# Kernel optimization log

Hardware: AMD Instinct MI355X
Metric: run time of the kernel (lower is better)

## Reference

```python
import jax, jax.numpy as jnp
import numpy as np
from jax import lax

T, H, I, E = 1024, 2048, 1024, 16
G, TOPK_GROUP, TOP_K = 4, 2, 4
ROUTED_SCALE = 2.5
W_SCALE = 0.02  # keep activations in a sane range


def setup_inputs() -> dict:
    key = jax.random.key(0)
    ks = jax.random.split(key, 7)
    return {
        "hidden_states": jax.random.normal(ks[0], (T, H), jnp.float32),
        "gate_w": jax.random.normal(ks[1], (E, H), jnp.float32) * W_SCALE,
        "e_bias": jax.random.normal(ks[2], (E,), jnp.float32),
        "w_gate_up": jax.random.normal(ks[3], (E, 2 * I, H), jnp.float32) * W_SCALE,
        "w_down": jax.random.normal(ks[4], (E, H, I), jnp.float32) * W_SCALE,
        "shared_w_gate_up": jax.random.normal(ks[5], (2 * I, H), jnp.float32) * W_SCALE,
        "shared_w_down": jax.random.normal(ks[6], (H, I), jnp.float32) * W_SCALE,
    }


def _grouped_topk(scores, e_bias):
    # scores: sigmoid router scores [T, E]
    scores_b = scores + e_bias[None, :]
    # group score = sum of top-2 biased scores within each group (bias branch)
    group_scores = jnp.sum(lax.top_k(scores_b.reshape(-1, G, E // G), 2)[0], axis=-1)  # [T, G]
    _, group_idx = lax.top_k(group_scores, TOPK_GROUP)  # [T, topk_group]
    group_mask = jnp.any(jax.nn.one_hot(group_idx, G, dtype=jnp.bool_), axis=1)  # [T, G]
    score_mask = jnp.repeat(group_mask, E // G, axis=-1)  # [T, E]
    tmp = jnp.where(score_mask, scores_b, 0.0)
    _, topk_ids = lax.top_k(tmp, TOP_K)  # [T, K]
    topk_w = jnp.take_along_axis(scores, topk_ids, axis=1)  # weights from UNbiased scores
    topk_w = topk_w / jnp.sum(topk_w, axis=-1, keepdims=True)  # renormalize
    return topk_w, topk_ids


def _silu_and_mul(gu):
    g, u = jnp.split(gu, 2, axis=-1)
    return jax.nn.silu(g) * u


def reference(hidden_states, gate_w, e_bias, w_gate_up, w_down,
              shared_w_gate_up, shared_w_down):
    x = hidden_states  # [T, H]
    # shared expert MLP
    shared = _silu_and_mul(x @ shared_w_gate_up.T) @ shared_w_down.T  # [T, H]
    # router
    logits = x @ gate_w.T                      # [T, E]
    scores = jax.nn.sigmoid(logits)
    topk_w, topk_ids = _grouped_topk(scores, e_bias)
    # dense combine weights [T, E] (zero for unselected experts)
    combine = jnp.zeros((T, E), x.dtype).at[jnp.arange(T)[:, None], topk_ids].add(topk_w)
    # routed experts: SwiGLU per expert, combined with routing weights
    gu = jnp.einsum('th,eih->tei', x, w_gate_up)        # [T, E, 2I]
    a = _silu_and_mul(gu)                               # [T, E, I]
    routed = jnp.einsum('tei,ehi,te->th', a, w_down, combine)  # [T, H]
    return routed * ROUTED_SCALE + shared
```

## Files before the change

### kernel.cpp

```cpp
#include <hip/hip_runtime.h>
#include <math.h>

typedef __bf16 bf16;
typedef bf16 bf16x4 __attribute__((ext_vector_type(4)));
typedef bf16 bf16x8 __attribute__((ext_vector_type(8)));
typedef float f32x4 __attribute__((ext_vector_type(4)));

#define T_TOK   1024
#define H_DIM   2048
#define I_DIM   1024
#define E_NUM   16
#define NPAIR_R 4096
#define NPAIR   5120

typedef __attribute__((address_space(3))) unsigned int lds_uint;
typedef __attribute__((address_space(1))) const unsigned int gbl_uint;
__device__ __forceinline__ void gld16(const void* g, void* l) {
  __builtin_amdgcn_global_load_lds((gbl_uint*)g, (lds_uint*)l, 16, 0, 0);
}

__global__ __launch_bounds__(256) void router_kernel(
    const float* __restrict__ x, const float* __restrict__ gate_w,
    const float* __restrict__ e_bias, bf16* __restrict__ xb,
    float* __restrict__ out,
    int* __restrict__ topk_ids, float* __restrict__ topk_w,
    int* __restrict__ counts)
{
  int t = blockIdx.x;
  int tid = threadIdx.x;
  float acc[16];
#pragma unroll
  for (int e = 0; e < 16; ++e) acc[e] = 0.f;
  const float* xr = x + (size_t)t * H_DIM;
  bf16* xbr = xb + (size_t)t * H_DIM;
  float* outr = out + (size_t)t * H_DIM;
  for (int h = tid; h < H_DIM; h += 256) {
    float xv = xr[h];
    xbr[h] = (bf16)xv;
    outr[h] = 0.f;
#pragma unroll
    for (int e = 0; e < 16; ++e) acc[e] += xv * gate_w[e * H_DIM + h];
  }
#pragma unroll
  for (int e = 0; e < 16; ++e) {
#pragma unroll
    for (int off = 32; off >= 1; off >>= 1)
      acc[e] += __shfl_down(acc[e], off, 64);
  }
  __shared__ float red[4][16];
  int lane = tid & 63, wave = tid >> 6;
  if (lane == 0) {
#pragma unroll
    for (int e = 0; e < 16; ++e) red[wave][e] = acc[e];
  }
  __syncthreads();
  if (tid == 0) {
    float scores[16], sb[16];
    for (int e = 0; e < 16; ++e) {
      float l = red[0][e] + red[1][e] + red[2][e] + red[3][e];
      float s = 1.f / (1.f + expf(-l));
      scores[e] = s;
      sb[e] = s + e_bias[e];
    }
    float gs[4];
    for (int g = 0; g < 4; ++g) {
      float b1 = -1e30f, b2 = -1e30f;
      for (int j = 0; j < 4; ++j) {
        float v = sb[g * 4 + j];
        if (v > b1) { b2 = b1; b1 = v; }
        else if (v > b2) b2 = v;
      }
      gs[g] = b1 + b2;
    }
    int g1 = 0; float bv = gs[0];
    for (int g = 1; g < 4; ++g) if (gs[g] > bv) { bv = gs[g]; g1 = g; }
    int g2 = -1; float bv2 = -1e30f;
    for (int g = 0; g < 4; ++g) if (g != g1 && gs[g] > bv2) { bv2 = gs[g]; g2 = g; }
    float tmp[16];
    for (int e = 0; e < 16; ++e) {
      int grp = e >> 2;
      tmp[e] = (grp == g1 || grp == g2) ? sb[e] : 0.0f;
    }
    bool used[16] = {false};
    int ids[4]; float wv[4]; float wsum = 0.f;
    for (int k = 0; k < 4; ++k) {
      int bi = 0; float bvv = -1e30f;
      for (int i = 0; i < 16; ++i)
        if (!used[i] && tmp[i] > bvv) { bvv = tmp[i]; bi = i; }
      used[bi] = true;
      ids[k] = bi; wv[k] = scores[bi]; wsum += scores[bi];
    }
    float inv = 1.f / wsum;
    for (int k = 0; k < 4; ++k) {
      topk_ids[t * 4 + k] = ids[k];
      topk_w[t * 4 + k] = wv[k] * inv;
      atomicAdd(&counts[ids[k]], 1);
    }
  }
}

__global__ __launch_bounds__(1024) void build_pairs_kernel(
    const int* __restrict__ topk_ids, const float* __restrict__ topk_w,
    const int* __restrict__ counts, int* __restrict__ off,
    int* __restrict__ pair_token, float* __restrict__ pair_scale)
{
  __shared__ int s_off[17];
  __shared__ int s_cur[16];
  int tid = threadIdx.x;
  if (tid == 0) {
    int s = 0;
    for (int e = 0; e < 16; ++e) { s_off[e] = s; off[e] = s; s += counts[e]; }
    s_off[16] = s; off[16] = s;
  }
  if (tid < 16) s_cur[tid] = 0;
  __syncthreads();
  for (int i = tid; i < NPAIR; i += 1024) {
    if (i < NPAIR_R) {
      int e = topk_ids[i];
      int pos = atomicAdd(&s_cur[e], 1);
      int idx = s_off[e] + pos;
      pair_token[idx] = i >> 2;
      pair_scale[idx] = 2.5f * topk_w[i];
    } else {
      pair_token[i] = i - NPAIR_R;
      pair_scale[i] = 1.0f;
    }
  }
}

__global__ __launch_bounds__(256, 2) void gateup_kernel(
    const bf16* __restrict__ xb, const float* __restrict__ w_gu,
    const float* __restrict__ s_wgu,
    const int* __restrict__ off, const int* __restrict__ pair_token,
    bf16* __restrict__ a_buf)
{
  const int nt = blockIdx.x;
  const int mt = blockIdx.y;
  const int e  = blockIdx.z;
  const int poff = (e < 16) ? off[e]     : NPAIR_R;
  const int pend = (e < 16) ? off[e + 1] : NPAIR;
  const int cnt  = pend - poff;
  if (mt * 128 >= cnt) return;
  const float* __restrict__ B = (e < 16) ? (w_gu + (size_t)e * 2 * I_DIM * H_DIM) : s_wgu;

  __shared__ __align__(16) bf16  As[3 * 4096];
  __shared__ __align__(16) float Bs[3 * 4096];

  const int tid = threadIdx.x;
  const int lane = tid & 63;
  const int wave = tid >> 6;
  const int wm = wave >> 1, wn = wave & 1;
  const int c0 = lane >> 4;
  const int fr = lane & 15;

  const bf16* aptr[2];
#pragma unroll
  for (int s = 0; s < 2; ++s) {
    int idx = s * 256 + tid;
    int ar = idx >> 2, ach = idx & 3;
    int sch = ach ^ ((ar >> 1) & 3);
    int p = poff + mt * 128 + ar;
    aptr[s] = xb + (size_t)pair_token[p] * H_DIM + sch * 8;
  }
  const float* bptr[4];
#pragma unroll
  for (int s = 0; s < 4; ++s) {
    int idx = s * 256 + tid;
    int br = idx >> 3, bch = idx & 7;
    int sch = bch ^ (br & 7);
    int rg = nt * 64 + br + (br >= 64 ? 960 : 0);
    bptr[s] = B + (size_t)rg * H_DIM + sch * 4;
  }
  int a_off[4];
#pragma unroll
  for (int mi = 0; mi < 4; ++mi) {
    int ar = wm * 64 + mi * 16 + fr;
    a_off[mi] = ar * 64 + ((c0 ^ ((ar >> 1) & 3)) << 4);
  }
  int b_off[4];
#pragma unroll
  for (int ni = 0; ni < 4; ++ni) {
    int br = wn * 32 + (ni & 1) * 16 + fr + (ni >> 1) * 64;
    b_off[ni] = br * 128 + (((2 * c0) ^ (br & 7)) << 4);
  }

  f32x4 acc[4][4];
  f32x4 zz = {0.f, 0.f, 0.f, 0.f};
#pragma unroll
  for (int mi = 0; mi < 4; ++mi)
#pragma unroll
    for (int ni = 0; ni < 4; ++ni) acc[mi][ni] = zz;

  const int ldso = tid * 16;
  auto stage = [&](int k0, int b) {
#pragma unroll
    for (int s = 0; s < 2; ++s)
      gld16(aptr[s] + k0, (char*)As + b * 8192 + s * 4096 + ldso);
#pragma unroll
    for (int s = 0; s < 4; ++s)
      gld16(bptr[s] + k0, (char*)Bs + b * 16384 + s * 4096 + ldso);
  };
  auto compute = [&](int b) {
    const char* Ab = (const char*)As + b * 8192;
    const char* Bb = (const char*)Bs + b * 16384;
    bf16x8 af[4], bv[4];
#pragma unroll
    for (int mi = 0; mi < 4; ++mi)
      af[mi] = *(const bf16x8*)(Ab + a_off[mi]);
#pragma unroll
    for (int ni = 0; ni < 4; ++ni) {
      f32x4 x0 = *(const f32x4*)(Bb + b_off[ni]);
      f32x4 x1 = *(const f32x4*)(Bb + (b_off[ni] ^ 16));
      bf16x8 t;
      t[0] = (bf16)x0[0]; t[1] = (bf16)x0[1]; t[2] = (bf16)x0[2]; t[3] = (bf16)x0[3];
      t[4] = (bf16)x1[0]; t[5] = (bf16)x1[1]; t[6] = (bf16)x1[2]; t[7] = (bf16)x1[3];
      bv[ni] = t;
    }
#pragma unroll
    for (int mi = 0; mi < 4; ++mi)
#pragma unroll
      for (int ni = 0; ni < 4; ++ni)
        acc[mi][ni] = __builtin_amdgcn_mfma_f32_16x16x32_bf16(af[mi], bv[ni], acc[mi][ni], 0, 0, 0);
  };

  const int NT = H_DIM / 32;
  stage(0, 0);
  stage(32, 1);
  int ca = 0, cb = 1, cc = 2;
  for (int t = 0; t + 2 < NT; ++t) {
    stage((t + 2) * 32, cc);
    asm volatile("s_waitcnt vmcnt(12)" ::: "memory");
    __builtin_amdgcn_s_barrier();
    compute(ca);
    asm volatile("" ::: "memory");
    __builtin_amdgcn_s_barrier();
    int tmp = ca; ca = cb; cb = cc; cc = tmp;
  }
  asm volatile("s_waitcnt vmcnt(6)" ::: "memory");
  __builtin_amdgcn_s_barrier();
  compute(ca);
  asm volatile("s_waitcnt vmcnt(0)" ::: "memory");
  __builtin_amdgcn_s_barrier();
  compute(cb);

#pragma unroll
  for (int mi = 0; mi < 4; ++mi) {
#pragma unroll
    for (int reg = 0; reg < 4; ++reg) {
      int r = wm * 64 + mi * 16 + c0 * 4 + reg;
      int rl = mt * 128 + r;
      if (rl < cnt) {
        size_t p = (size_t)(poff + rl);
        bf16* orow = a_buf + p * I_DIM + nt * 64 + wn * 32 + fr;
#pragma unroll
        for (int ni = 0; ni < 2; ++ni) {
          float g = acc[mi][ni][reg];
          float u = acc[mi][ni + 2][reg];
          float sg = g / (1.f + expf(-g));
          orow[ni * 16] = (bf16)(sg * u);
        }
      }
    }
  }
}

__global__ __launch_bounds__(256, 2) void down_kernel(
    const bf16* __restrict__ a_buf, const float* __restrict__ w_dn,
    const float* __restrict__ s_wdn,
    const int* __restrict__ off, const int* __restrict__ pair_token,
    const float* __restrict__ pair_scale, float* __restrict__ out)
{
  const int nt = blockIdx.x;
  const int mt = blockIdx.y;
  const int e  = blockIdx.z;
  const int poff = (e < 16) ? off[e]     : NPAIR_R;
  const int pend = (e < 16) ? off[e + 1] : NPAIR;
  const int cnt  = pend - poff;
  if (mt * 128 >= cnt) return;
  const float* __restrict__ B = (e < 16) ? (w_dn + (size_t)e * H_DIM * I_DIM) : s_wdn;

  __shared__ __align__(16) bf16  As[3 * 4096];
  __shared__ __align__(16) float Bs[3 * 4096];

  const int tid = threadIdx.x;
  const int lane = tid & 63;
  const int wave = tid >> 6;
  const int wm = wave >> 1, wn = wave & 1;
  const int c0 = lane >> 4;
  const int fr = lane & 15;

  const bf16* aptr[2];
#pragma unroll
  for (int s = 0; s < 2; ++s) {
    int idx = s * 256 + tid;
    int ar = idx >> 2, ach = idx & 3;
    int sch = ach ^ ((ar >> 1) & 3);
    int p = poff + mt * 128 + ar;
    aptr[s] = a_buf + (size_t)p * I_DIM + sch * 8;
  }
  const float* bptr[4];
#pragma unroll
  for (int s = 0; s < 4; ++s) {
    int idx = s * 256 + tid;
    int br = idx >> 3, bch = idx & 7;
    int sch = bch ^ (br & 7);
    bptr[s] = B + (size_t)(nt * 128 + br) * I_DIM + sch * 4;
  }
  int a_off[4];
#pragma unroll
  for (int mi = 0; mi < 4; ++mi) {
    int ar = wm * 64 + mi * 16 + fr;
    a_off[mi] = ar * 64 + ((c0 ^ ((ar >> 1) & 3)) << 4);
  }
  int b_off[4];
#pragma unroll
  for (int ni = 0; ni < 4; ++ni) {
    int br = wn * 64 + ni * 16 + fr;
    b_off[ni] = br * 128 + (((2 * c0) ^ (br & 7)) << 4);
  }

  f32x4 acc[4][4];
  f32x4 zz = {0.f, 0.f, 0.f, 0.f};
#pragma unroll
  for (int mi = 0; mi < 4; ++mi)
#pragma unroll
    for (int ni = 0; ni < 4; ++ni) acc[mi][ni] = zz;

  const int ldso = tid * 16;
  auto stage = [&](int k0, int b) {
#pragma unroll
    for (int s = 0; s < 2; ++s)
      gld16(aptr[s] + k0, (char*)As + b * 8192 + s * 4096 + ldso);
#pragma unroll
    for (int s = 0; s < 4; ++s)
      gld16(bptr[s] + k0, (char*)Bs + b * 16384 + s * 4096 + ldso);
  };
  auto compute = [&](int b) {
    const char* Ab = (const char*)As + b * 8192;
    const char* Bb = (const char*)Bs + b * 16384;
    bf16x8 af[4], bv[4];
#pragma unroll
    for (int mi = 0; mi < 4; ++mi)
      af[mi] = *(const bf16x8*)(Ab + a_off[mi]);
#pragma unroll
    for (int ni = 0; ni < 4; ++ni) {
      f32x4 x0 = *(const f32x4*)(Bb + b_off[ni]);
      f32x4 x1 = *(const f32x4*)(Bb + (b_off[ni] ^ 16));
      bf16x8 t;
      t[0] = (bf16)x0[0]; t[1] = (bf16)x0[1]; t[2] = (bf16)x0[2]; t[3] = (bf16)x0[3];
      t[4] = (bf16)x1[0]; t[5] = (bf16)x1[1]; t[6] = (bf16)x1[2]; t[7] = (bf16)x1[3];
      bv[ni] = t;
    }
#pragma unroll
    for (int mi = 0; mi < 4; ++mi)
#pragma unroll
      for (int ni = 0; ni < 4; ++ni)
        acc[mi][ni] = __builtin_amdgcn_mfma_f32_16x16x32_bf16(af[mi], bv[ni], acc[mi][ni], 0, 0, 0);
  };

  const int NT = I_DIM / 32;
  stage(0, 0);
  stage(32, 1);
  int ca = 0, cb = 1, cc = 2;
  for (int t = 0; t + 2 < NT; ++t) {
    stage((t + 2) * 32, cc);
    asm volatile("s_waitcnt vmcnt(12)" ::: "memory");
    __builtin_amdgcn_s_barrier();
    compute(ca);
    asm volatile("" ::: "memory");
    __builtin_amdgcn_s_barrier();
    int tmp = ca; ca = cb; cb = cc; cc = tmp;
  }
  asm volatile("s_waitcnt vmcnt(6)" ::: "memory");
  __builtin_amdgcn_s_barrier();
  compute(ca);
  asm volatile("s_waitcnt vmcnt(0)" ::: "memory");
  __builtin_amdgcn_s_barrier();
  compute(cb);

  const int colb = nt * 128 + wn * 64;
#pragma unroll
  for (int mi = 0; mi < 4; ++mi) {
#pragma unroll
    for (int reg = 0; reg < 4; ++reg) {
      int r = wm * 64 + mi * 16 + c0 * 4 + reg;
      int rl = mt * 128 + r;
      if (rl < cnt) {
        int p = poff + rl;
        int tok = pair_token[p];
        float sc = pair_scale[p];
        float* orow = out + (size_t)tok * H_DIM + colb + fr;
#pragma unroll
        for (int ni = 0; ni < 4; ++ni)
          atomicAdd(&orow[ni * 16], acc[mi][ni][reg] * sc);
      }
    }
  }
}

extern "C" void kernel_launch(void* const* d_in, const int* in_sizes, int n_in,
                              void* d_out, int out_size, void* d_ws, size_t ws_size,
                              hipStream_t stream)
{
  const float* x     = (const float*)d_in[0];
  const float* gatew = (const float*)d_in[1];
  const float* ebias = (const float*)d_in[2];
  const float* w_gu  = (const float*)d_in[3];
  const float* w_dn  = (const float*)d_in[4];
  const float* s_wgu = (const float*)d_in[5];
  const float* s_wdn = (const float*)d_in[6];
  float* out = (float*)d_out;

  char* ws = (char*)d_ws;
  int*   off        = (int*)(ws + 0);
  int*   counts     = (int*)(ws + 128);
  int*   topk_ids   = (int*)(ws + 256);
  float* topk_w     = (float*)(ws + 16640);
  int*   pair_token = (int*)(ws + 33024);
  float* pair_scale = (float*)(ws + 53504);
  bf16*  x_bf16     = (bf16*)(ws + 73984);
  bf16*  a_buf      = (bf16*)(ws + 73984 + 4194304);

  hipMemsetAsync(ws + 128, 0, 64, stream);

  router_kernel<<<T_TOK, 256, 0, stream>>>(x, gatew, ebias, x_bf16, out,
                                           topk_ids, topk_w, counts);
  build_pairs_kernel<<<1, 1024, 0, stream>>>(topk_ids, topk_w, counts, off,
                                             pair_token, pair_scale);
  dim3 g1(16, 8, 17);
  gateup_kernel<<<g1, 256, 0, stream>>>(x_bf16, w_gu, s_wgu, off, pair_token, a_buf);
  dim3 g2(16, 8, 17);
  down_kernel<<<g2, 256, 0, stream>>>(a_buf, w_dn, s_wdn, off, pair_token, pair_scale, out);
}
```

Baseline: 666.4 us.

## Enlarge MoE GEMM M-tiles to 256 rows with 512-thread blocks and batch router tokens

The gate-up and down expert GEMMs now use 512-thread blocks that cover 256 pair rows instead of 128, and the pipeline drops from triple to double buffering. The grid is reordered so each expert's M-tiles are adjacent. Each fp32 weight tile is therefore loaded once per 256 rows rather than per 128, which roughly halves weight streaming from HBM. The router kernel now handles four tokens per block so each gate_w load is reused across those tokens. The trade-offs are shallower prefetch, more idle rows on experts with few tokens, and fewer blocks in flight.

Measured after the change: 711.2 us. +6.7%, slower.

```diff
diff --git a/kernel.cpp b/kernel.cpp
--- a/kernel.cpp
+++ b/kernel.cpp
@@ -26,38 +26,51 @@
     int* __restrict__ topk_ids, float* __restrict__ topk_w,
     int* __restrict__ counts)
 {
-  int t = blockIdx.x;
-  int tid = threadIdx.x;
-  float acc[16];
-#pragma unroll
-  for (int e = 0; e < 16; ++e) acc[e] = 0.f;
-  const float* xr = x + (size_t)t * H_DIM;
-  bf16* xbr = xb + (size_t)t * H_DIM;
-  float* outr = out + (size_t)t * H_DIM;
+  const int blk = blockIdx.x;
+  const int tid = threadIdx.x;
+  const int t0 = blk * 4;
+  float acc[4][16];
+#pragma unroll
+  for (int tt = 0; tt < 4; ++tt)
+#pragma unroll
+    for (int e = 0; e < 16; ++e) acc[tt][e] = 0.f;
+
   for (int h = tid; h < H_DIM; h += 256) {
-    float xv = xr[h];
-    xbr[h] = (bf16)xv;
-    outr[h] = 0.f;
-#pragma unroll
-    for (int e = 0; e < 16; ++e) acc[e] += xv * gate_w[e * H_DIM + h];
-  }
-#pragma unroll
-  for (int e = 0; e < 16; ++e) {
-#pragma unroll
-    for (int off = 32; off >= 1; off >>= 1)
-      acc[e] += __shfl_down(acc[e], off, 64);
-  }
-  __shared__ float red[4][16];
+    float gw[16];
+#pragma unroll
+    for (int e = 0; e < 16; ++e) gw[e] = gate_w[e * H_DIM + h];
+#pragma unroll
+    for (int tt = 0; tt < 4; ++tt) {
+      float xv = x[(size_t)(t0 + tt) * H_DIM + h];
+      xb[(size_t)(t0 + tt) * H_DIM + h] = (bf16)xv;
+      out[(size_t)(t0 + tt) * H_DIM + h] = 0.f;
+#pragma unroll
+      for (int e = 0; e < 16; ++e) acc[tt][e] += xv * gw[e];
+    }
+  }
+#pragma unroll
+  for (int tt = 0; tt < 4; ++tt)
+#pragma unroll
+    for (int e = 0; e < 16; ++e) {
+#pragma unroll
+      for (int off = 32; off >= 1; off >>= 1)
+        acc[tt][e] += __shfl_down(acc[tt][e], off, 64);
+    }
+  __shared__ float red[4][4][16];
   int lane = tid & 63, wave = tid >> 6;
   if (lane == 0) {
 #pragma unroll
-    for (int e = 0; e < 16; ++e) red[wave][e] = acc[e];
+    for (int tt = 0; tt < 4; ++tt)
+#pragma unroll
+      for (int e = 0; e < 16; ++e) red[wave][tt][e] = acc[tt][e];
   }
   __syncthreads();
-  if (tid == 0) {
+  if (tid < 4) {
+    const int tt = tid;
+    const int t = t0 + tt;
     float scores[16], sb[16];
     for (int e = 0; e < 16; ++e) {
-      float l = red[0][e] + red[1][e] + red[2][e] + red[3][e];
+      float l = red[0][tt][e] + red[1][tt][e] + red[2][tt][e] + red[3][tt][e];
       float s = 1.f / (1.f + expf(-l));
       scores[e] = s;
       sb[e] = s + e_bias[e];
@@ -128,44 +141,47 @@
   }
 }
 
-__global__ __launch_bounds__(256, 2) void gateup_kernel(
+__global__ __launch_bounds__(512, 4) void gateup_kernel(
     const bf16* __restrict__ xb, const float* __restrict__ w_gu,
     const float* __restrict__ s_wgu,
     const int* __restrict__ off, const int* __restrict__ pair_token,
     bf16* __restrict__ a_buf)
 {
-  const int nt = blockIdx.x;
-  const int mt = blockIdx.y;
-  const int e  = blockIdx.z;
+  const int g = blockIdx.x;
+  if (g >= 68) return;
+  const int e  = g >> 2;
+  const int mt = g & 3;
+  const int nt = blockIdx.y;
   const int poff = (e < 16) ? off[e]     : NPAIR_R;
   const int pend = (e < 16) ? off[e + 1] : NPAIR;
   const int cnt  = pend - poff;
-  if (mt * 128 >= cnt) return;
+  if (mt * 256 >= cnt) return;
   const float* __restrict__ B = (e < 16) ? (w_gu + (size_t)e * 2 * I_DIM * H_DIM) : s_wgu;
 
-  __shared__ __align__(16) bf16  As[3 * 4096];
-  __shared__ __align__(16) float Bs[3 * 4096];
+  __shared__ __align__(16) bf16  As[2 * 8192];
+  __shared__ __align__(16) float Bs[2 * 4096];
 
   const int tid = threadIdx.x;
   const int lane = tid & 63;
   const int wave = tid >> 6;
-  const int wm = wave >> 1, wn = wave & 1;
+  const int wm = wave >> 1;
+  const int wn = wave & 1;
   const int c0 = lane >> 4;
   const int fr = lane & 15;
 
   const bf16* aptr[2];
 #pragma unroll
   for (int s = 0; s < 2; ++s) {
-    int idx = s * 256 + tid;
+    int idx = s * 512 + tid;
     int ar = idx >> 2, ach = idx & 3;
     int sch = ach ^ ((ar >> 1) & 3);
-    int p = poff + mt * 128 + ar;
+    int p = poff + mt * 256 + ar;
     aptr[s] = xb + (size_t)pair_token[p] * H_DIM + sch * 8;
   }
-  const float* bptr[4];
-#pragma unroll
-  for (int s = 0; s < 4; ++s) {
-    int idx = s * 256 + tid;
+  const float* bptr[2];
+#pragma unroll
+  for (int s = 0; s < 2; ++s) {
+    int idx = s * 512 + tid;
     int br = idx >> 3, bch = idx & 7;
     int sch = bch ^ (br & 7);
     int rg = nt * 64 + br + (br >= 64 ? 960 : 0);
@@ -195,13 +211,13 @@
   auto stage = [&](int k0, int b) {
 #pragma unroll
     for (int s = 0; s < 2; ++s)
-      gld16(aptr[s] + k0, (char*)As + b * 8192 + s * 4096 + ldso);
-#pragma unroll
-    for (int s = 0; s < 4; ++s)
-      gld16(bptr[s] + k0, (char*)Bs + b * 16384 + s * 4096 + ldso);
+      gld16(aptr[s] + k0, (char*)As + b * 16384 + s * 8192 + ldso);
+#pragma unroll
+    for (int s = 0; s < 2; ++s)
+      gld16(bptr[s] + k0, (char*)Bs + b * 16384 + s * 8192 + ldso);
   };
   auto compute = [&](int b) {
-    const char* Ab = (const char*)As + b * 8192;
+    const char* Ab = (const char*)As + b * 16384;
     const char* Bb = (const char*)Bs + b * 16384;
     bf16x8 af[4], bv[4];
 #pragma unroll
@@ -225,83 +241,82 @@
 
   const int NT = H_DIM / 32;
   stage(0, 0);
-  stage(32, 1);
-  int ca = 0, cb = 1, cc = 2;
-  for (int t = 0; t + 2 < NT; ++t) {
-    stage((t + 2) * 32, cc);
-    asm volatile("s_waitcnt vmcnt(12)" ::: "memory");
+  int cur = 0;
+  for (int t = 0; t < NT - 1; ++t) {
+    stage((t + 1) * 32, cur ^ 1);
+    asm volatile("s_waitcnt vmcnt(4)" ::: "memory");
     __builtin_amdgcn_s_barrier();
-    compute(ca);
+    compute(cur);
     asm volatile("" ::: "memory");
     __builtin_amdgcn_s_barrier();
-    int tmp = ca; ca = cb; cb = cc; cc = tmp;
-  }
-  asm volatile("s_waitcnt vmcnt(6)" ::: "memory");
-  __builtin_amdgcn_s_barrier();
-  compute(ca);
+    cur ^= 1;
+  }
   asm volatile("s_waitcnt vmcnt(0)" ::: "memory");
   __builtin_amdgcn_s_barrier();
-  compute(cb);
+  compute(cur);
 
 #pragma unroll
   for (int mi = 0; mi < 4; ++mi) {
 #pragma unroll
     for (int reg = 0; reg < 4; ++reg) {
       int r = wm * 64 + mi * 16 + c0 * 4 + reg;
-      int rl = mt * 128 + r;
+      int rl = mt * 256 + r;
       if (rl < cnt) {
         size_t p = (size_t)(poff + rl);
         bf16* orow = a_buf + p * I_DIM + nt * 64 + wn * 32 + fr;
 #pragma unroll
         for (int ni = 0; ni < 2; ++ni) {
-          float g = acc[mi][ni][reg];
-          float u = acc[mi][ni + 2][reg];
-          float sg = g / (1.f + expf(-g));
-          orow[ni * 16] = (bf16)(sg * u);
+          float gg = acc[mi][ni][reg];
+          float uu = acc[mi][ni + 2][reg];
+          float sg = gg / (1.f + expf(-gg));
+          orow[ni * 16] = (bf16)(sg * uu);
         }
       }
     }
   }
 }
 
-__global__ __launch_bounds__(256, 2) void down_kernel(
+__global__ __launch_bounds__(512, 4) void down_kernel(
     const bf16* __restrict__ a_buf, const float* __restrict__ w_dn,
     const float* __restrict__ s_wdn,
     const int* __restrict__ off, const int* __restrict__ pair_token,
     const float* __restrict__ pair_scale, float* __restrict__ out)
 {
-  const int nt = blockIdx.x;
-  const int mt = blockIdx.y;
-  const int e  = blockIdx.z;
+  const int g = blockIdx.x;
+  if (g >= 68) return;
+  const int e  = g >> 2;
+  const int mt = g & 3;
+  const int nt = blockIdx.y;
   const int poff = (e < 16) ? off[e]     : NPAIR_R;
   const int pend = (e < 16) ? off[e + 1] : NPAIR;
   const int cnt  = pend - poff;
-  if (mt * 128 >= cnt) return;
+  if (mt * 256 >= cnt) return;
   const float* __restrict__ B = (e < 16) ? (w_dn + (size_t)e * H_DIM * I_DIM) : s_wdn;
 
-  __shared__ __align__(16) bf16  As[3 * 4096];
-  __shared__ __align__(16) float Bs[3 * 4096];
+  __shared__ __align__(16) bf16  As[2 * 8192];
+  __shared__ __align__(16) float Bs[2 * 4096];
 
   const int tid = threadIdx.x;
   const int lane = tid & 63;
   const int wave = tid >> 6;
-  const int wm = wave >> 1, wn = wave & 1;
+  const int wm = wave >> 1;
+  const int wn = wave & 1;
   const int c0 = lane >> 4;
   const int fr = lane & 15;
 
   const bf16* aptr[2];
 #pragma unroll
   for (int s = 0; s < 2; ++s) {
-    int idx = s * 256 + tid;
+    int idx = s * 512 + tid;
     int ar = idx >> 2, ach = idx & 3;
     int sch = ach ^ ((ar >> 1) & 3);
-    int p = poff + mt * 128 + ar;
+    int p = poff + mt * 256 + ar;
     aptr[s] = a_buf + (size_t)p * I_DIM + sch * 8;
   }
-  const float* bptr[4];
-#pragma unroll
-  for (int s = 0; s < 4; ++s) {
-    int idx = s * 256 + tid;
+  const float* bptr[2];
+#pragma unroll
+  for (int s = 0; s < 2; ++s) {
+    int idx = s * 512 + tid;
     int br = idx >> 3, bch = idx & 7;
     int sch = bch ^ (br & 7);
     bptr[s] = B + (size_t)(nt * 128 + br) * I_DIM + sch * 4;
@@ -330,13 +345,13 @@
   auto stage = [&](int k0, int b) {
 #pragma unroll
     for (int s = 0; s < 2; ++s)
-      gld16(aptr[s] + k0, (char*)As + b * 8192 + s * 4096 + ldso);
-#pragma unroll
-    for (int s = 0; s < 4; ++s)
-      gld16(bptr[s] + k0, (char*)Bs + b * 16384 + s * 4096 + ldso);
+      gld16(aptr[s] + k0, (char*)As + b * 16384 + s * 8192 + ldso);
+#pragma unroll
+    for (int s = 0; s < 2; ++s)
+      gld16(bptr[s] + k0, (char*)Bs + b * 16384 + s * 8192 + ldso);
   };
   auto compute = [&](int b) {
-    const char* Ab = (const char*)As + b * 8192;
+    const char* Ab = (const char*)As + b * 16384;
     const char* Bb = (const char*)Bs + b * 16384;
     bf16x8 af[4], bv[4];
 #pragma unroll
@@ -360,23 +375,19 @@
 
   const int NT = I_DIM / 32;
   stage(0, 0);
-  stage(32, 1);
-  int ca = 0, cb = 1, cc = 2;
-  for (int t = 0; t + 2 < NT; ++t) {
-    stage((t + 2) * 32, cc);
-    asm volatile("s_waitcnt vmcnt(12)" ::: "memory");
+  int cur = 0;
+  for (int t = 0; t < NT - 1; ++t) {
+    stage((t + 1) * 32, cur ^ 1);
+    asm volatile("s_waitcnt vmcnt(4)" ::: "memory");
     __builtin_amdgcn_s_barrier();
-    compute(ca);
+    compute(cur);
     asm volatile("" ::: "memory");
     __builtin_amdgcn_s_barrier();
-    int tmp = ca; ca = cb; cb = cc; cc = tmp;
-  }
-  asm volatile("s_waitcnt vmcnt(6)" ::: "memory");
-  __builtin_amdgcn_s_barrier();
-  compute(ca);
+    cur ^= 1;
+  }
   asm volatile("s_waitcnt vmcnt(0)" ::: "memory");
   __builtin_amdgcn_s_barrier();
-  compute(cb);
+  compute(cur);
 
   const int colb = nt * 128 + wn * 64;
 #pragma unroll
@@ -384,7 +395,7 @@
 #pragma unroll
     for (int reg = 0; reg < 4; ++reg) {
       int r = wm * 64 + mi * 16 + c0 * 4 + reg;
-      int rl = mt * 128 + r;
+      int rl = mt * 256 + r;
       if (rl < cnt) {
         int p = poff + rl;
         int tok = pair_token[p];
@@ -423,12 +434,11 @@
 
   hipMemsetAsync(ws + 128, 0, 64, stream);
 
-  router_kernel<<<T_TOK, 256, 0, stream>>>(x, gatew, ebias, x_bf16, out,
-                                           topk_ids, topk_w, counts);
+  router_kernel<<<T_TOK / 4, 256, 0, stream>>>(x, gatew, ebias, x_bf16, out,
+                                               topk_ids, topk_w, counts);
   build_pairs_kernel<<<1, 1024, 0, stream>>>(topk_ids, topk_w, counts, off,
                                              pair_token, pair_scale);
-  dim3 g1(16, 8, 17);
-  gateup_kernel<<<g1, 256, 0, stream>>>(x_bf16, w_gu, s_wgu, off, pair_token, a_buf);
-  dim3 g2(16, 8, 17);
-  down_kernel<<<g2, 256, 0, stream>>>(a_buf, w_dn, s_wdn, off, pair_token, pair_scale, out);
-}
+  dim3 gg(72, 16, 1);
+  gateup_kernel<<<gg, 512, 0, stream>>>(x_bf16, w_gu, s_wgu, off, pair_token, a_buf);
+  down_kernel<<<gg, 512, 0, stream>>>(a_buf, w_dn, s_wdn, off, pair_token, pair_scale, out);
+}
```
